# Kernel optimization log

Measured on AMD Instinct MI355X. Metric: run time of the kernel, lower is better.

## Reference

```python
import jax, jax.numpy as jnp
import numpy as np

N_POINTS = 2_000_000
OUTPUT_DIM = 8
L_RES = 128
H_RES = 1024


def _to_idx(c, size):
    # c in [-1, 1], align_corners=True mapping to pixel coords
    p = (c + 1.0) * 0.5 * (size - 1)
    i0 = jnp.floor(p)
    w = p - i0  # interpolation weight toward i1
    i0 = jnp.clip(i0.astype(jnp.int32), 0, size - 1)
    i1 = jnp.clip(i0 + 1, 0, size - 1)
    return i0, i1, w


def trilinear_sample(grid, coords):
    # grid: [C, D, H, W]; coords: [N, 3] with (x->W, y->H, z->D); returns [C, N]
    C, D, H, W = grid.shape
    x0, x1, wx = _to_idx(coords[:, 0], W)
    y0, y1, wy = _to_idx(coords[:, 1], H)
    z0, z1, wz = _to_idx(coords[:, 2], D)
    g = lambda zi, yi, xi: grid[:, zi, yi, xi]  # gather -> [C, N]
    out = (g(z0, y0, x0) * ((1 - wz) * (1 - wy) * (1 - wx))
           + g(z0, y0, x1) * ((1 - wz) * (1 - wy) * wx)
           + g(z0, y1, x0) * ((1 - wz) * wy * (1 - wx))
           + g(z0, y1, x1) * ((1 - wz) * wy * wx)
           + g(z1, y0, x0) * (wz * (1 - wy) * (1 - wx))
           + g(z1, y0, x1) * (wz * (1 - wy) * wx)
           + g(z1, y1, x0) * (wz * wy * (1 - wx))
           + g(z1, y1, x1) * (wz * wy * wx))
    return out


def bilinear_sample(plane, coords):
    # plane: [C, H, W]; coords: [N, 2] with (x->W, y->H); returns [C, N]
    C, H, W = plane.shape
    x0, x1, wx = _to_idx(coords[:, 0], W)
    y0, y1, wy = _to_idx(coords[:, 1], H)
    g = lambda yi, xi: plane[:, yi, xi]  # [C, N]
    out = (g(y0, x0) * ((1 - wy) * (1 - wx))
           + g(y0, x1) * ((1 - wy) * wx)
           + g(y1, x0) * (wy * (1 - wx))
           + g(y1, x1) * (wy * wx))
    return out


def setup_inputs() -> dict:
    key = jax.random.key(0)
    k1, k2, k3 = jax.random.split(key, 3)
    xyz = jax.random.uniform(k1, (N_POINTS, 3), dtype=jnp.float32)  # in [0,1) subset of [-1,1]
    L_grid = jax.random.normal(k2, (1, OUTPUT_DIM, L_RES, L_RES, L_RES), dtype=jnp.float32) * 0.1
    H_planes = jax.random.normal(k3, (3, OUTPUT_DIM, H_RES, H_RES), dtype=jnp.float32) * 0.1
    return {"xyz": xyz, "bound": 1, "L_grid": L_grid, "H_planes": H_planes}


def reference(xyz, bound, L_grid, H_planes):
    xyz_norm = xyz / bound  # [N, 3]
    L_out = trilinear_sample(L_grid[0], xyz_norm)  # [C, N]
    H_out = (bilinear_sample(H_planes[0], xyz_norm[:, jnp.array([0, 1])])
             + bilinear_sample(H_planes[1], xyz_norm[:, jnp.array([1, 2])])
             + bilinear_sample(H_planes[2], xyz_norm[:, jnp.array([2, 0])]))
    return (L_out + H_out).T  # [N, C]
```

## Files before the change

kernel.cpp:

```cpp
#include <hip/hip_runtime.h>

#define LRES 128
#define HRES 1024
#define CB 16
#define NC (CB * CB * CB)
#define NBSORT 256
#define BT 256

static const int LVOX = LRES * LRES * LRES;
static const int PPIX = HRES * HRES;


__device__ __forceinline__ void to_idx(float c, int size, int& i0, int& i1, float& w) {
    float p = (c + 1.0f) * 0.5f * (float)(size - 1);
    float f = floorf(p);
    w = p - f;
    int i = (int)f;
    i0 = min(max(i, 0), size - 1);
    i1 = min(i0 + 1, size - 1);
}

__device__ __forceinline__ unsigned f2bf(float f) {
    unsigned u = __float_as_uint(f);
    return (u + 0x7FFFu + ((u >> 16) & 1u)) >> 16;
}
__device__ __forceinline__ float bflo(unsigned u) { return __uint_as_float(u << 16); }
__device__ __forceinline__ float bfhi(unsigned u) { return __uint_as_float(u & 0xFFFF0000u); }

__device__ __forceinline__ void fma8u(float4& a0, float4& a1, uint4 q, float w) {
    a0.x = fmaf(bflo(q.x), w, a0.x);
    a0.y = fmaf(bfhi(q.x), w, a0.y);
    a0.z = fmaf(bflo(q.y), w, a0.z);
    a0.w = fmaf(bfhi(q.y), w, a0.w);
    a1.x = fmaf(bflo(q.z), w, a1.x);
    a1.y = fmaf(bfhi(q.z), w, a1.y);
    a1.z = fmaf(bflo(q.w), w, a1.z);
    a1.w = fmaf(bfhi(q.w), w, a1.w);
}

__device__ __forceinline__ unsigned spread3(unsigned x) {
    x &= 0x3FFu;
    x = (x | (x << 16)) & 0x030000FFu;
    x = (x | (x << 8)) & 0x0300F00Fu;
    x = (x | (x << 4)) & 0x030C30C3u;
    x = (x | (x << 2)) & 0x09249249u;
    return x;
}
__device__ __forceinline__ unsigned cell16(float x, float y, float z) {
    int cx = min(max((int)(x * (float)CB), 0), CB - 1);
    int cy = min(max((int)(y * (float)CB), 0), CB - 1);
    int cz = min(max((int)(z * (float)CB), 0), CB - 1);
    return spread3(cx) | (spread3(cy) << 1) | (spread3(cz) << 2);
}

__global__ __launch_bounds__(256) void transpose_bf(const float* __restrict__ src,
                                                    uint4* __restrict__ dst, int V) {
    int v = blockIdx.x * blockDim.x + threadIdx.x;
    if (v >= V) return;
    unsigned h[8];
#pragma unroll
    for (int c = 0; c < 8; ++c) h[c] = f2bf(src[(size_t)c * V + v]);
    uint4 o;
    o.x = h[0] | (h[1] << 16);
    o.y = h[2] | (h[3] << 16);
    o.z = h[4] | (h[5] << 16);
    o.w = h[6] | (h[7] << 16);
    dst[v] = o;
}


__global__ __launch_bounds__(BT) void hist_pb(const float* __restrict__ xyz,
                                              const int* __restrict__ boundp,
                                              unsigned* __restrict__ histmat, int N) {
    __shared__ unsigned h[NC];
    for (int i = threadIdx.x; i < NC; i += BT) h[i] = 0u;
    __syncthreads();
    float invb = 1.0f / (float)boundp[0];
    for (int n = blockIdx.x * BT + threadIdx.x; n < N; n += NBSORT * BT) {
        float x = xyz[(size_t)3 * n + 0] * invb;
        float y = xyz[(size_t)3 * n + 1] * invb;
        float z = xyz[(size_t)3 * n + 2] * invb;
        atomicAdd(&h[cell16(x, y, z)], 1u);
    }
    __syncthreads();
    unsigned* row = histmat + (size_t)blockIdx.x * NC;
    for (int i = threadIdx.x; i < NC; i += BT) row[i] = h[i];
}

__global__ __launch_bounds__(256) void rowpref(unsigned* __restrict__ histmat,
                                               unsigned* __restrict__ total) {
    int c = blockIdx.x * 256 + threadIdx.x;
    unsigned run = 0;
    for (int b = 0; b < NBSORT; ++b) {
        unsigned v = histmat[(size_t)b * NC + c];
        histmat[(size_t)b * NC + c] = run;
        run += v;
    }
    total[c] = run;
}

__global__ __launch_bounds__(1024) void scan2_k(const unsigned* __restrict__ total,
                                                unsigned* __restrict__ cellbase) {
    __shared__ unsigned s[1024];
    int tid = threadIdx.x;
    unsigned v[4];
    unsigned sum = 0;
#pragma unroll
    for (int k = 0; k < 4; ++k) {
        v[k] = total[tid * 4 + k];
        sum += v[k];
    }
    s[tid] = sum;
    __syncthreads();
    for (int o = 1; o < 1024; o <<= 1) {
        unsigned t = (tid >= o) ? s[tid - o] : 0u;
        __syncthreads();
        s[tid] += t;
        __syncthreads();
    }
    unsigned base = s[tid] - sum;
#pragma unroll
    for (int k = 0; k < 4; ++k) {
        cellbase[tid * 4 + k] = base;
        base += v[k];
    }
}

__global__ __launch_bounds__(BT) void scatter_pb(const float* __restrict__ xyz,
                                                 const int* __restrict__ boundp,
                                                 const unsigned* __restrict__ histmat,
                                                 const unsigned* __restrict__ cellbase,
                                                 float4* __restrict__ sorted, int N) {
    __shared__ unsigned cnt[NC];
    const unsigned* row = histmat + (size_t)blockIdx.x * NC;
    for (int i = threadIdx.x; i < NC; i += BT) cnt[i] = cellbase[i] + row[i];
    __syncthreads();
    float invb = 1.0f / (float)boundp[0];
    for (int n = blockIdx.x * BT + threadIdx.x; n < N; n += NBSORT * BT) {
        float x = xyz[(size_t)3 * n + 0] * invb;
        float y = xyz[(size_t)3 * n + 1] * invb;
        float z = xyz[(size_t)3 * n + 2] * invb;
        unsigned c = cell16(x, y, z);
        unsigned d = atomicAdd(&cnt[c], 1u);
        sorted[d] = make_float4(x, y, z, __int_as_float(n));
    }
}

__global__ __launch_bounds__(256) void sample_srt(const float4* __restrict__ sorted,
                                                  const uint4* __restrict__ gclb,
                                                  const uint4* __restrict__ pclb,
                                                  float* __restrict__ out, int N) {
    int i = blockIdx.x * blockDim.x + threadIdx.x;
    if (i >= N) return;
    float4 rec = sorted[i];
    float x = rec.x, y = rec.y, z = rec.z;
    int idx = __float_as_int(rec.w);

    int x0, x1, y0, y1, z0, z1;
    float wx, wy, wz;
    to_idx(x, LRES, x0, x1, wx);
    to_idx(y, LRES, y0, y1, wy);
    to_idx(z, LRES, z0, z1, wz);
    const uint4* b00 = gclb + ((size_t)z0 * LRES + y0) * LRES;
    const uint4* b01 = gclb + ((size_t)z0 * LRES + y1) * LRES;
    const uint4* b10 = gclb + ((size_t)z1 * LRES + y0) * LRES;
    const uint4* b11 = gclb + ((size_t)z1 * LRES + y1) * LRES;
    uint4 g0 = b00[x0], g1 = b00[x1], g2 = b01[x0], g3 = b01[x1];
    uint4 g4 = b10[x0], g5 = b10[x1], g6 = b11[x0], g7 = b11[x1];

    const float cw[3] = {x, y, z};
    const float ch[3] = {y, z, x};
    float pww[3], pwh[3];
    uint4 r[12];
#pragma unroll
    for (int p = 0; p < 3; ++p) {
        int w0, w1, h0, h1;
        to_idx(cw[p], HRES, w0, w1, pww[p]);
        to_idx(ch[p], HRES, h0, h1, pwh[p]);
        const uint4* base = pclb + (size_t)p * PPIX;
        const uint4* r0 = base + (size_t)h0 * HRES;
        const uint4* r1 = base + (size_t)h1 * HRES;
        r[4 * p + 0] = r0[w0];
        r[4 * p + 1] = r0[w1];
        r[4 * p + 2] = r1[w0];
        r[4 * p + 3] = r1[w1];
    }

    float4 a0 = make_float4(0.f, 0.f, 0.f, 0.f);
    float4 a1 = make_float4(0.f, 0.f, 0.f, 0.f);
    {
        float ux = 1.f - wx, uy = 1.f - wy, uz = 1.f - wz;
        fma8u(a0, a1, g0, uz * uy * ux);
        fma8u(a0, a1, g1, uz * uy * wx);
        fma8u(a0, a1, g2, uz * wy * ux);
        fma8u(a0, a1, g3, uz * wy * wx);
        fma8u(a0, a1, g4, wz * uy * ux);
        fma8u(a0, a1, g5, wz * uy * wx);
        fma8u(a0, a1, g6, wz * wy * ux);
        fma8u(a0, a1, g7, wz * wy * wx);
    }
#pragma unroll
    for (int p = 0; p < 3; ++p) {
        float ww = pww[p], wh = pwh[p];
        float uw = 1.f - ww, uh = 1.f - wh;
        fma8u(a0, a1, r[4 * p + 0], uh * uw);
        fma8u(a0, a1, r[4 * p + 1], uh * ww);
        fma8u(a0, a1, r[4 * p + 2], wh * uw);
        fma8u(a0, a1, r[4 * p + 3], wh * ww);
    }

    float4* o = (float4*)(out + (size_t)idx * 8);
    o[0] = a0;
    o[1] = a1;
}

__global__ __launch_bounds__(256) void sample_cf(
    const float* __restrict__ xyz, const int* __restrict__ boundp,
    const float* __restrict__ Lg, const float* __restrict__ Hp,
    float* __restrict__ out, int N) {
    int n = blockIdx.x * blockDim.x + threadIdx.x;
    if (n >= N) return;
    float invb = 1.0f / (float)boundp[0];
    float x = xyz[(size_t)3 * n + 0] * invb;
    float y = xyz[(size_t)3 * n + 1] * invb;
    float z = xyz[(size_t)3 * n + 2] * invb;
    float acc[8];
#pragma unroll
    for (int c = 0; c < 8; ++c) acc[c] = 0.f;
    {
        int x0, x1, y0, y1, z0, z1;
        float wx, wy, wz;
        to_idx(x, LRES, x0, x1, wx);
        to_idx(y, LRES, y0, y1, wy);
        to_idx(z, LRES, z0, z1, wz);
        float ux = 1.f - wx, uy = 1.f - wy, uz = 1.f - wz;
        size_t i8[8];
        i8[0] = ((size_t)z0 * LRES + y0) * LRES + x0;
        i8[1] = ((size_t)z0 * LRES + y0) * LRES + x1;
        i8[2] = ((size_t)z0 * LRES + y1) * LRES + x0;
        i8[3] = ((size_t)z0 * LRES + y1) * LRES + x1;
        i8[4] = ((size_t)z1 * LRES + y0) * LRES + x0;
        i8[5] = ((size_t)z1 * LRES + y0) * LRES + x1;
        i8[6] = ((size_t)z1 * LRES + y1) * LRES + x0;
        i8[7] = ((size_t)z1 * LRES + y1) * LRES + x1;
        float w8[8] = {uz * uy * ux, uz * uy * wx, uz * wy * ux, uz * wy * wx,
                       wz * uy * ux, wz * uy * wx, wz * wy * ux, wz * wy * wx};
#pragma unroll
        for (int c = 0; c < 8; ++c) {
            const float* g = Lg + (size_t)c * LVOX;
            float s = 0.f;
#pragma unroll
            for (int k = 0; k < 8; ++k) s = fmaf(g[i8[k]], w8[k], s);
            acc[c] += s;
        }
    }
    {
        const float cw[3] = {x, y, z};
        const float ch[3] = {y, z, x};
        for (int p = 0; p < 3; ++p) {
            int w0, w1, h0, h1;
            float ww, wh;
            to_idx(cw[p], HRES, w0, w1, ww);
            to_idx(ch[p], HRES, h0, h1, wh);
            float uw = 1.f - ww, uh = 1.f - wh;
            size_t i4[4] = {(size_t)h0 * HRES + w0, (size_t)h0 * HRES + w1,
                            (size_t)h1 * HRES + w0, (size_t)h1 * HRES + w1};
            float w4[4] = {uh * uw, uh * ww, wh * uw, wh * ww};
            const float* pb = Hp + (size_t)p * 8 * PPIX;
#pragma unroll
            for (int c = 0; c < 8; ++c) {
                const float* g = pb + (size_t)c * PPIX;
                float s = 0.f;
#pragma unroll
                for (int k = 0; k < 4; ++k) s = fmaf(g[i4[k]], w4[k], s);
                acc[c] += s;
            }
        }
    }
#pragma unroll
    for (int c = 0; c < 8; ++c) out[(size_t)n * 8 + c] = acc[c];
}

extern "C" void kernel_launch(void* const* d_in, const int* in_sizes, int n_in,
                              void* d_out, int out_size, void* d_ws, size_t ws_size,
                              hipStream_t stream) {
    const float* xyz = (const float*)d_in[0];
    const int* bound = (const int*)d_in[1];
    const float* Lg = (const float*)d_in[2];
    const float* Hp = (const float*)d_in[3];
    float* out = (float*)d_out;
    int N = in_sizes[0] / 3;

    size_t off = 0;
    size_t gclb_b = (size_t)LVOX * 16;
    size_t pclb_b = (size_t)3 * PPIX * 16;
    size_t sort_b = (size_t)N * 16;
    size_t hmat_b = (size_t)NBSORT * NC * 4;
    size_t tot_b = (size_t)NC * 4;
    size_t cb_b = (size_t)NC * 4;
    size_t need = gclb_b + pclb_b + sort_b + hmat_b + tot_b + cb_b;

    if (ws_size >= need) {
        char* w = (char*)d_ws;
        uint4* gclb = (uint4*)(w + off);        off += gclb_b;
        uint4* pclb = (uint4*)(w + off);        off += pclb_b;
        float4* sorted = (float4*)(w + off);    off += sort_b;
        unsigned* hmat = (unsigned*)(w + off);  off += hmat_b;
        unsigned* total = (unsigned*)(w + off); off += tot_b;
        unsigned* cbase = (unsigned*)(w + off);

        transpose_bf<<<(LVOX + 255) / 256, 256, 0, stream>>>(Lg, gclb, LVOX);
        for (int p = 0; p < 3; ++p) {
            transpose_bf<<<(PPIX + 255) / 256, 256, 0, stream>>>(
                Hp + (size_t)p * 8 * PPIX, pclb + (size_t)p * PPIX, PPIX);
        }
        hist_pb<<<NBSORT, BT, 0, stream>>>(xyz, bound, hmat, N);
        rowpref<<<NC / 256, 256, 0, stream>>>(hmat, total);
        scan2_k<<<1, 1024, 0, stream>>>(total, cbase);
        scatter_pb<<<NBSORT, BT, 0, stream>>>(xyz, bound, hmat, cbase, sorted, N);
        sample_srt<<<(N + 255) / 256, 256, 0, stream>>>(sorted, gclb, pclb, out, N);
    } else {
        sample_cf<<<(N + 255) / 256, 256, 0, stream>>>(xyz, bound, Lg, Hp, out, N);
    }
}
```

Before: 410.3 us.

## Fuse grid bf16 transposes with histogram into one prep kernel, transpose histmat layout

Merges the four grid/plane bf16 transpose launches and the histogram pass into a single prep kernel, so the sort histogram runs alongside the conversion work and there are fewer launches. The histogram matrix is stored cell-major so the row prefix kernel reads each cell's 256 block counts contiguously with vector loads instead of strided ones. Sort and scatter blocks grow to 1024 threads, and nontemporal loads and stores are used for the converted grids, sorted records and outputs. The risks are that the scatter writes to histmat become strided, and that nontemporal stores on the gathered grids may keep them out of cache for the sampling kernel that reads them next.

```diff
diff --git a/kernel.cpp b/kernel.cpp
--- a/kernel.cpp
+++ b/kernel.cpp
@@ -5,10 +5,14 @@
 #define CB 16
 #define NC (CB * CB * CB)
 #define NBSORT 256
-#define BT 256
+#define BTS 1024
 
 static const int LVOX = LRES * LRES * LRES;
 static const int PPIX = HRES * HRES;
+static const int TV = LVOX + 3 * PPIX;
+
+typedef float f32x4 __attribute__((ext_vector_type(4)));
+typedef unsigned u32x4 __attribute__((ext_vector_type(4)));
 
 
 __device__ __forceinline__ void to_idx(float c, int size, int& i0, int& i1, float& w) {
@@ -27,7 +31,7 @@
 __device__ __forceinline__ float bflo(unsigned u) { return __uint_as_float(u << 16); }
 __device__ __forceinline__ float bfhi(unsigned u) { return __uint_as_float(u & 0xFFFF0000u); }
 
-__device__ __forceinline__ void fma8u(float4& a0, float4& a1, uint4 q, float w) {
+__device__ __forceinline__ void fma8u(f32x4& a0, f32x4& a1, uint4 q, float w) {
     a0.x = fmaf(bflo(q.x), w, a0.x);
     a0.y = fmaf(bfhi(q.x), w, a0.y);
     a0.z = fmaf(bflo(q.y), w, a0.z);
@@ -53,48 +57,69 @@
     return spread3(cx) | (spread3(cy) << 1) | (spread3(cz) << 2);
 }
 
-__global__ __launch_bounds__(256) void transpose_bf(const float* __restrict__ src,
-                                                    uint4* __restrict__ dst, int V) {
-    int v = blockIdx.x * blockDim.x + threadIdx.x;
-    if (v >= V) return;
-    unsigned h[8];
-#pragma unroll
-    for (int c = 0; c < 8; ++c) h[c] = f2bf(src[(size_t)c * V + v]);
-    uint4 o;
-    o.x = h[0] | (h[1] << 16);
-    o.y = h[2] | (h[3] << 16);
-    o.z = h[4] | (h[5] << 16);
-    o.w = h[6] | (h[7] << 16);
-    dst[v] = o;
-}
-
-
-__global__ __launch_bounds__(BT) void hist_pb(const float* __restrict__ xyz,
+__global__ __launch_bounds__(BTS) void prep_k(const float* __restrict__ xyz,
                                               const int* __restrict__ boundp,
-                                              unsigned* __restrict__ histmat, int N) {
+                                              const float* __restrict__ Lg,
+                                              const float* __restrict__ Hp,
+                                              unsigned* __restrict__ histmat,
+                                              u32x4* __restrict__ gclb,
+                                              u32x4* __restrict__ pclb, int N) {
     __shared__ unsigned h[NC];
-    for (int i = threadIdx.x; i < NC; i += BT) h[i] = 0u;
-    __syncthreads();
-    float invb = 1.0f / (float)boundp[0];
-    for (int n = blockIdx.x * BT + threadIdx.x; n < N; n += NBSORT * BT) {
-        float x = xyz[(size_t)3 * n + 0] * invb;
-        float y = xyz[(size_t)3 * n + 1] * invb;
-        float z = xyz[(size_t)3 * n + 2] * invb;
-        atomicAdd(&h[cell16(x, y, z)], 1u);
-    }
-    __syncthreads();
-    unsigned* row = histmat + (size_t)blockIdx.x * NC;
-    for (int i = threadIdx.x; i < NC; i += BT) row[i] = h[i];
+    int b = blockIdx.x;
+    if (b < NBSORT) {
+        for (int i = threadIdx.x; i < NC; i += BTS) h[i] = 0u;
+        __syncthreads();
+        float invb = 1.0f / (float)boundp[0];
+        for (int n = b * BTS + threadIdx.x; n < N; n += NBSORT * BTS) {
+            float x = xyz[(size_t)3 * n + 0] * invb;
+            float y = xyz[(size_t)3 * n + 1] * invb;
+            float z = xyz[(size_t)3 * n + 2] * invb;
+            atomicAdd(&h[cell16(x, y, z)], 1u);
+        }
+        __syncthreads();
+        for (int i = threadIdx.x; i < NC; i += BTS)
+            histmat[(size_t)i * NBSORT + b] = h[i];
+    } else {
+        int v = (b - NBSORT) * BTS + threadIdx.x;
+        if (v >= TV) return;
+        unsigned hh[8];
+        u32x4* dst;
+        if (v < LVOX) {
+#pragma unroll
+            for (int c = 0; c < 8; ++c) hh[c] = f2bf(Lg[(size_t)c * LVOX + v]);
+            dst = gclb + v;
+        } else {
+            int u = v - LVOX;
+            int p = u >> 20;
+            int r = u & (PPIX - 1);
+            const float* src = Hp + (size_t)p * 8 * PPIX;
+#pragma unroll
+            for (int c = 0; c < 8; ++c) hh[c] = f2bf(src[(size_t)c * PPIX + r]);
+            dst = pclb + (size_t)p * PPIX + r;
+        }
+        u32x4 o;
+        o.x = hh[0] | (hh[1] << 16);
+        o.y = hh[2] | (hh[3] << 16);
+        o.z = hh[4] | (hh[5] << 16);
+        o.w = hh[6] | (hh[7] << 16);
+        __builtin_nontemporal_store(o, dst);
+    }
 }
 
 __global__ __launch_bounds__(256) void rowpref(unsigned* __restrict__ histmat,
                                                unsigned* __restrict__ total) {
     int c = blockIdx.x * 256 + threadIdx.x;
+    u32x4* row = (u32x4*)(histmat + (size_t)c * NBSORT);
     unsigned run = 0;
-    for (int b = 0; b < NBSORT; ++b) {
-        unsigned v = histmat[(size_t)b * NC + c];
-        histmat[(size_t)b * NC + c] = run;
-        run += v;
+#pragma unroll 4
+    for (int k = 0; k < NBSORT / 4; ++k) {
+        u32x4 v = row[k];
+        unsigned t;
+        t = v.x; v.x = run; run += t;
+        t = v.y; v.y = run; run += t;
+        t = v.z; v.z = run; run += t;
+        t = v.w; v.w = run; run += t;
+        row[k] = v;
     }
     total[c] = run;
 }
@@ -126,17 +151,18 @@
     }
 }
 
-__global__ __launch_bounds__(BT) void scatter_pb(const float* __restrict__ xyz,
-                                                 const int* __restrict__ boundp,
-                                                 const unsigned* __restrict__ histmat,
-                                                 const unsigned* __restrict__ cellbase,
-                                                 float4* __restrict__ sorted, int N) {
+__global__ __launch_bounds__(BTS) void scatter_pb(const float* __restrict__ xyz,
+                                                  const int* __restrict__ boundp,
+                                                  const unsigned* __restrict__ histmat,
+                                                  const unsigned* __restrict__ cellbase,
+                                                  float4* __restrict__ sorted, int N) {
     __shared__ unsigned cnt[NC];
-    const unsigned* row = histmat + (size_t)blockIdx.x * NC;
-    for (int i = threadIdx.x; i < NC; i += BT) cnt[i] = cellbase[i] + row[i];
+    int b = blockIdx.x;
+    for (int i = threadIdx.x; i < NC; i += BTS)
+        cnt[i] = cellbase[i] + histmat[(size_t)i * NBSORT + b];
     __syncthreads();
     float invb = 1.0f / (float)boundp[0];
-    for (int n = blockIdx.x * BT + threadIdx.x; n < N; n += NBSORT * BT) {
+    for (int n = b * BTS + threadIdx.x; n < N; n += NBSORT * BTS) {
         float x = xyz[(size_t)3 * n + 0] * invb;
         float y = xyz[(size_t)3 * n + 1] * invb;
         float z = xyz[(size_t)3 * n + 2] * invb;
@@ -146,13 +172,13 @@
     }
 }
 
-__global__ __launch_bounds__(256) void sample_srt(const float4* __restrict__ sorted,
+__global__ __launch_bounds__(256) void sample_srt(const f32x4* __restrict__ sorted,
                                                   const uint4* __restrict__ gclb,
                                                   const uint4* __restrict__ pclb,
                                                   float* __restrict__ out, int N) {
     int i = blockIdx.x * blockDim.x + threadIdx.x;
     if (i >= N) return;
-    float4 rec = sorted[i];
+    f32x4 rec = __builtin_nontemporal_load(sorted + i);
     float x = rec.x, y = rec.y, z = rec.z;
     int idx = __float_as_int(rec.w);
 
@@ -186,8 +212,8 @@
         r[4 * p + 3] = r1[w1];
     }
 
-    float4 a0 = make_float4(0.f, 0.f, 0.f, 0.f);
-    float4 a1 = make_float4(0.f, 0.f, 0.f, 0.f);
+    f32x4 a0 = (f32x4)0.f;
+    f32x4 a1 = (f32x4)0.f;
     {
         float ux = 1.f - wx, uy = 1.f - wy, uz = 1.f - wz;
         fma8u(a0, a1, g0, uz * uy * ux);
@@ -209,9 +235,9 @@
         fma8u(a0, a1, r[4 * p + 3], wh * ww);
     }
 
-    float4* o = (float4*)(out + (size_t)idx * 8);
-    o[0] = a0;
-    o[1] = a1;
+    f32x4* o = (f32x4*)(out + (size_t)idx * 8);
+    __builtin_nontemporal_store(a0, o);
+    __builtin_nontemporal_store(a1, o + 1);
 }
 
 __global__ __launch_bounds__(256) void sample_cf(
@@ -295,30 +321,28 @@
     size_t gclb_b = (size_t)LVOX * 16;
     size_t pclb_b = (size_t)3 * PPIX * 16;
     size_t sort_b = (size_t)N * 16;
-    size_t hmat_b = (size_t)NBSORT * NC * 4;
+    size_t hmat_b = (size_t)NC * NBSORT * 4;
     size_t tot_b = (size_t)NC * 4;
     size_t cb_b = (size_t)NC * 4;
     size_t need = gclb_b + pclb_b + sort_b + hmat_b + tot_b + cb_b;
 
     if (ws_size >= need) {
         char* w = (char*)d_ws;
-        uint4* gclb = (uint4*)(w + off);        off += gclb_b;
-        uint4* pclb = (uint4*)(w + off);        off += pclb_b;
+        u32x4* gclb = (u32x4*)(w + off);        off += gclb_b;
+        u32x4* pclb = (u32x4*)(w + off);        off += pclb_b;
         float4* sorted = (float4*)(w + off);    off += sort_b;
         unsigned* hmat = (unsigned*)(w + off);  off += hmat_b;
         unsigned* total = (unsigned*)(w + off); off += tot_b;
         unsigned* cbase = (unsigned*)(w + off);
 
-        transpose_bf<<<(LVOX + 255) / 256, 256, 0, stream>>>(Lg, gclb, LVOX);
-        for (int p = 0; p < 3; ++p) {
-            transpose_bf<<<(PPIX + 255) / 256, 256, 0, stream>>>(
-                Hp + (size_t)p * 8 * PPIX, pclb + (size_t)p * PPIX, PPIX);
-        }
-        hist_pb<<<NBSORT, BT, 0, stream>>>(xyz, bound, hmat, N);
+        int prep_blocks = NBSORT + (TV + BTS - 1) / BTS;
+        prep_k<<<prep_blocks, BTS, 0, stream>>>(xyz, bound, Lg, Hp, hmat, gclb, pclb, N);
         rowpref<<<NC / 256, 256, 0, stream>>>(hmat, total);
         scan2_k<<<1, 1024, 0, stream>>>(total, cbase);
-        scatter_pb<<<NBSORT, BT, 0, stream>>>(xyz, bound, hmat, cbase, sorted, N);
-        sample_srt<<<(N + 255) / 256, 256, 0, stream>>>(sorted, gclb, pclb, out, N);
+        scatter_pb<<<NBSORT, BTS, 0, stream>>>(xyz, bound, hmat, cbase, sorted, N);
+        sample_srt<<<(N + 255) / 256, 256, 0, stream>>>((const f32x4*)sorted,
+                                                        (const uint4*)gclb,
+                                                        (const uint4*)pclb, out, N);
     } else {
         sample_cf<<<(N + 255) / 256, 256, 0, stream>>>(xyz, bound, Lg, Hp, out, N);
     }
```

Result: slower. 483.5 us (+17.8%).
